# Optimization experiments

Measured on AMD Instinct MI355X. Metric: run time of the kernel, lower is better.

## Reference

```python
import jax, jax.numpy as jnp
import numpy as np

V, H, NH, I, L, P = 32000, 1024, 16, 4096, 8, 2048
B, S = 2, 2048
DH = H // NH
EPS = 1e-5


def setup_inputs() -> dict:
    key = jax.random.key(0)
    ks = jax.random.split(key, 12)
    std = 0.02
    inp = {
        'input_ids': jax.random.randint(ks[0], (B, S), 0, V),
        'attention_mask': jnp.ones((B, S), dtype=jnp.float32),
        'tok_emb': jax.random.normal(ks[1], (V, H), jnp.float32) * std,
        'pos_emb': jax.random.normal(ks[2], (P, H), jnp.float32) * std,
        # per-layer params stacked on leading L dim (torch Linear convention: y = x @ W.T + b)
        'Wq': jax.random.normal(ks[3], (L, H, H), jnp.float32) * std,
        'bq': jnp.zeros((L, H), jnp.float32),
        'Wk': jax.random.normal(ks[4], (L, H, H), jnp.float32) * std,
        'bk': jnp.zeros((L, H), jnp.float32),
        'Wv': jax.random.normal(ks[5], (L, H, H), jnp.float32) * std,
        'bv': jnp.zeros((L, H), jnp.float32),
        'Wi': jax.random.normal(ks[6], (L, I, H), jnp.float32) * std,
        'bi': jnp.zeros((L, I), jnp.float32),
        'Wo': jax.random.normal(ks[7], (L, H, I), jnp.float32) * std,
        'bo': jnp.zeros((L, H), jnp.float32),
        'ln1_g': jnp.ones((L, H), jnp.float32),
        'ln1_b': jnp.zeros((L, H), jnp.float32),
        'ln2_g': jnp.ones((L, H), jnp.float32),
        'ln2_b': jnp.zeros((L, H), jnp.float32),
        'lnf_g': jnp.ones((H,), jnp.float32),
        'lnf_b': jnp.zeros((H,), jnp.float32),
        'Wlm': jax.random.normal(ks[8], (V, H), jnp.float32) * std,
    }
    return inp


def _layer_norm(x, g, b):
    m = jnp.mean(x, axis=-1, keepdims=True)
    v = jnp.var(x, axis=-1, keepdims=True)
    return (x - m) * jax.lax.rsqrt(v + EPS) * g + b


def reference(input_ids, attention_mask, tok_emb, pos_emb, Wq, bq, Wk, bk, Wv, bv,
              Wi, bi, Wo, bo, ln1_g, ln1_b, ln2_g, ln2_b, lnf_g, lnf_b, Wlm):
    b, s = input_ids.shape
    h = tok_emb[input_ids] + pos_emb[jnp.arange(s)][None, :, :]  # [B,S,H]
    mask = (1.0 - attention_mask)[:, None, None, :] * -10000.0   # [B,1,1,S]
    scale = 1.0 / (DH ** 0.5)

    def split_heads(x):  # [B,S,H] -> [B,NH,S,DH]
        return x.reshape(b, s, NH, DH).transpose(0, 2, 1, 3)

    def block(h, p):
        wq, bq_, wk, bk_, wv, bv_, wi, bi_, wo, bo_, g1, b1, g2, b2 = p
        q = split_heads(h @ wq.T + bq_)
        k = split_heads(h @ wk.T + bk_)
        v = split_heads(h @ wv.T + bv_)
        scores = jnp.einsum('bhqd,bhkd->bhqk', q, k) * scale + mask
        probs = jax.nn.softmax(scores, axis=-1)
        ctx = jnp.einsum('bhqk,bhkd->bhqd', probs, v)
        ctx = ctx.transpose(0, 2, 1, 3).reshape(b, s, H)
        h1 = _layer_norm(h + ctx, g1, b1)
        mlp = jax.nn.gelu(h1 @ wi.T + bi_, approximate=False) @ wo.T + bo_
        return _layer_norm(h1 + mlp, g2, b2), None

    h, _ = jax.lax.scan(block, h, (Wq, bq, Wk, bk, Wv, bv, Wi, bi, Wo, bo,
                                   ln1_g, ln1_b, ln2_g, ln2_b))
    h = _layer_norm(h, lnf_g, lnf_b)
    return h @ Wlm.T  # [B,S,V]
```

## Files before the change

### kernel.cpp

```cpp
#include <hip/hip_runtime.h>
#include <hip/hip_bf16.h>

#define V_ 32000
#define H_ 1024
#define NH_ 16
#define I_ 4096
#define L_ 8
#define B_ 2
#define S_ 2048
#define DH_ 64
#define M_ 4096
#define QS_ 3072

typedef __attribute__((ext_vector_type(4))) float f32x4;
typedef __attribute__((ext_vector_type(8))) short s16x8;

#define BARRIER() do { asm volatile("" ::: "memory"); __builtin_amdgcn_s_barrier(); asm volatile("" ::: "memory"); } while (0)
#define SCHEDB()  __builtin_amdgcn_sched_barrier(0)

__device__ __forceinline__ unsigned short f2b(float f) {
  union { float f; unsigned u; } x; x.f = f;
  return (unsigned short)((x.u + 0x7FFFu + ((x.u >> 16) & 1u)) >> 16);
}

__device__ __forceinline__ void gl_lds16(const unsigned short* g, unsigned short* l) {
  __builtin_amdgcn_global_load_lds(
      (__attribute__((address_space(1))) const void*)g,
      (__attribute__((address_space(3))) void*)l, 16, 0, 0);
}

__global__ __launch_bounds__(256) void wcvt(const float* __restrict__ src,
                                            unsigned short* __restrict__ dst) {
  size_t i = ((size_t)blockIdx.x * 256 + threadIdx.x) * 4;
  float4 v = *(const float4*)(src + i);
  ushort4 b;
  b.x = f2b(v.x); b.y = f2b(v.y); b.z = f2b(v.z); b.w = f2b(v.w);
  *(ushort4*)(dst + i) = b;
}

__global__ __launch_bounds__(256) void qkvcat_all(const float* __restrict__ q,
                                                  const float* __restrict__ k,
                                                  const float* __restrict__ v,
                                                  unsigned short* __restrict__ dst) {
  size_t i = ((size_t)blockIdx.x * 256 + threadIdx.x) * 4;
  size_t l = i / (3u * H_ * H_);
  size_t r = i - l * (3u * H_ * H_);
  const float* s; size_t off;
  if (r < (size_t)H_ * H_)          { s = q; off = l * H_ * H_ + r; }
  else if (r < 2u * H_ * H_)        { s = k; off = l * H_ * H_ + r - (size_t)H_ * H_; }
  else                              { s = v; off = l * H_ * H_ + r - 2u * H_ * H_; }
  float4 vv = *(const float4*)(s + off);
  ushort4 b;
  b.x = f2b(vv.x); b.y = f2b(vv.y); b.z = f2b(vv.z); b.w = f2b(vv.w);
  *(ushort4*)(dst + i) = b;
}

__global__ __launch_bounds__(256) void qkvcat(const float* __restrict__ q,
                                              const float* __restrict__ k,
                                              const float* __restrict__ v,
                                              unsigned short* __restrict__ dst) {
  int i = (blockIdx.x * 256 + threadIdx.x) * 4;
  const float* s; int off;
  if (i < H_ * H_)          { s = q; off = i; }
  else if (i < 2 * H_ * H_) { s = k; off = i - H_ * H_; }
  else                      { s = v; off = i - 2 * H_ * H_; }
  float4 vv = *(const float4*)(s + off);
  ushort4 b;
  b.x = f2b(vv.x); b.y = f2b(vv.y); b.z = f2b(vv.z); b.w = f2b(vv.w);
  *(ushort4*)(dst + i) = b;
}

__global__ __launch_bounds__(256) void bcat(const float* __restrict__ bq,
                                            const float* __restrict__ bk,
                                            const float* __restrict__ bv,
                                            float* __restrict__ dst) {
  int i = blockIdx.x * 256 + threadIdx.x;
  int l = i / (3 * H_), r = i - l * 3 * H_;
  int p = r >> 10, c = r & (H_ - 1);
  const float* s = (p == 0) ? bq : ((p == 1) ? bk : bv);
  dst[i] = s[l * H_ + c];
}

__global__ __launch_bounds__(256) void embed_kernel(
    const int* __restrict__ ids, const float* __restrict__ tok,
    const float* __restrict__ pos, float* __restrict__ h,
    unsigned short* __restrict__ xbf)
{
  int row = blockIdx.x;
  int c4 = threadIdx.x;
  int id = ids[row];
  int s = row & (S_ - 1);
  float4 tv = ((const float4*)(tok + (size_t)id * H_))[c4];
  float4 pv = ((const float4*)(pos + (size_t)s * H_))[c4];
  float4 v; v.x = tv.x + pv.x; v.y = tv.y + pv.y; v.z = tv.z + pv.z; v.w = tv.w + pv.w;
  ((float4*)(h + (size_t)row * H_))[c4] = v;
  ushort4 b; b.x = f2b(v.x); b.y = f2b(v.y); b.z = f2b(v.z); b.w = f2b(v.w);
  ((ushort4*)(xbf + (size_t)row * H_))[c4] = b;
}

template<int EPI>
__global__ __launch_bounds__(256) void gemm_bt(
    const unsigned short* __restrict__ A, const unsigned short* __restrict__ Wb,
    const float* __restrict__ bias, float* __restrict__ outf,
    unsigned short* __restrict__ outb, int M, int N, int K, int ksz)
{
  __shared__ unsigned short As[2][128][32];
  __shared__ unsigned short Bs[2][128][32];
  int t = threadIdx.x;
  int lane = t & 63, wid = t >> 6;
  int m0 = blockIdx.x * 128, n0 = blockIdx.y * 128;
  int z = blockIdx.z;
  int koff = z * ksz;
  const float* bz = (z == 0) ? bias : nullptr;
  if (EPI == 0) outf += (size_t)z * M * N;
  int wm = (wid >> 1) * 64, wn = (wid & 1) * 64;
  int fr = lane & 15, hi = lane >> 4;
  int lrow = lane >> 2;
  int lcolsw = (((lane & 3) ^ (lrow & 3)) * 8);
  int ke = ((hi ^ (fr & 3)) * 8);

  f32x4 acc[4][4] = {};

  const unsigned short* Abase = A  + (size_t)(m0 + wid * 32 + lrow) * K + lcolsw;
  const unsigned short* Bbase = Wb + (size_t)(n0 + wid * 32 + lrow) * K + lcolsw;

  auto stage = [&](int s, int k0) {
    gl_lds16(Abase + k0,                  &As[s][wid * 32][0]);
    gl_lds16(Abase + k0 + (size_t)16 * K, &As[s][wid * 32 + 16][0]);
    gl_lds16(Bbase + k0,                  &Bs[s][wid * 32][0]);
    gl_lds16(Bbase + k0 + (size_t)16 * K, &Bs[s][wid * 32 + 16][0]);
  };

  stage(0, koff);

  int cur = 0;
  for (int k0 = koff; k0 < koff + ksz; k0 += 32) {
    asm volatile("s_waitcnt vmcnt(0)" ::: "memory");
    BARRIER();
    if (k0 + 32 < koff + ksz) stage(cur ^ 1, k0 + 32);
    SCHEDB();
    s16x8 af[4], bfr[4];
    #pragma unroll
    for (int i = 0; i < 4; ++i) af[i]  = *(const s16x8*)(&As[cur][wm + i * 16 + fr][ke]);
    #pragma unroll
    for (int j = 0; j < 4; ++j) bfr[j] = *(const s16x8*)(&Bs[cur][wn + j * 16 + fr][ke]);
    #pragma unroll
    for (int i = 0; i < 4; ++i)
      #pragma unroll
      for (int j = 0; j < 4; ++j)
        acc[i][j] = __builtin_amdgcn_mfma_f32_16x16x32_bf16(af[i], bfr[j], acc[i][j], 0, 0, 0);
    cur ^= 1;
  }

  int fq = lane >> 4;
  #pragma unroll
  for (int i = 0; i < 4; ++i) {
    #pragma unroll
    for (int j = 0; j < 4; ++j) {
      #pragma unroll
      for (int r = 0; r < 4; ++r) {
        int row = m0 + wm + i * 16 + fq * 4 + r;
        int col = n0 + wn + j * 16 + fr;
        float v = acc[i][j][r] + (bz ? bz[col] : 0.f);
        if (EPI == 0) {
          outf[(size_t)row * N + col] = v;
        } else if (EPI == 1) {
          float ge = 0.5f * v * (1.0f + erff(v * 0.70710678118f));
          outb[(size_t)row * N + col] = f2b(ge);
        } else {
          outb[(size_t)row * N + col] = f2b(v);
        }
      }
    }
  }
}

template<int EPI>
__global__ __launch_bounds__(512, 2) void gemm256(
    const unsigned short* __restrict__ A, const unsigned short* __restrict__ Wb,
    const float* __restrict__ bias, float* __restrict__ outf,
    unsigned short* __restrict__ outb, int M, int N, int K)
{
  __shared__ unsigned short ASm[2][16384];
  __shared__ unsigned short BSm[2][16384];

  const int t = threadIdx.x;
  const int lane = t & 63, wid = t >> 6;
  const int wm = wid >> 2, wn = wid & 3;
  const int fr = lane & 15, hi = lane >> 4;

  const int Nt = N >> 8;
  const int nwg = gridDim.x;
  const int cpx = nwg >> 3;
  int bid = (int)blockIdx.x;
  int swz = (bid & 7) * cpx + (bid >> 3);
  int band = swz / (4 * Nt);
  int rem = swz - band * (4 * Nt);
  const int m0 = (band * 4 + (rem & 3)) << 8;
  const int n0 = (rem >> 2) << 8;

  const int NT = K >> 6;

  const int srow = lane >> 3;
  const int scol = ((lane & 7) ^ srow) << 3;
  const int ch0 = wid * 2;

  const int axorb = (fr & 7) << 4;
  const int koe0 = ((hi * 16) ^ axorb) >> 1;
  const int koe1 = (((hi * 16) | 64) ^ axorb) >> 1;

  f32x4 acc[8][4] = {};

  auto stage_half = [&](int slot, int h, int k0) {
    if (h < 2) {
      const unsigned short* src =
          A + (size_t)(m0 + h * 128 + ch0 * 8 + srow) * K + k0 + scol;
      unsigned short* dst = &ASm[slot][(h * 128 + ch0 * 8) * 64];
      gl_lds16(src, dst);
      gl_lds16(src + (size_t)8 * K, dst + 8 * 64);
    } else {
      const unsigned short* src =
          Wb + (size_t)(n0 + (h - 2) * 128 + ch0 * 8 + srow) * K + k0 + scol;
      unsigned short* dst = &BSm[slot][((h - 2) * 128 + ch0 * 8) * 64];
      gl_lds16(src, dst);
      gl_lds16(src + (size_t)8 * K, dst + 8 * 64);
    }
  };

  stage_half(0, 2, 0); stage_half(0, 3, 0); stage_half(0, 0, 0); stage_half(0, 1, 0);

  s16x8 af0[4][2], af1[4][2], bfv[4][2];

  for (int T = 0; T < NT; ++T) {
    const int s = T & 1;
    const int k1 = (T + 1) << 6;
    const bool more = (T + 1 < NT);

    asm volatile("s_waitcnt vmcnt(0)" ::: "memory");
    BARRIER();

    const unsigned short* As_ = ASm[s];
    const unsigned short* Bs_ = BSm[s];

    #pragma unroll
    for (int mi = 0; mi < 4; ++mi) {
      const unsigned short* p = As_ + (wm * 128 + mi * 16 + fr) * 64;
      af0[mi][0] = *(const s16x8*)(p + koe0);
      af0[mi][1] = *(const s16x8*)(p + koe1);
    }
    #pragma unroll
    for (int nj = 0; nj < 4; ++nj) {
      const unsigned short* p = Bs_ + (wn * 64 + nj * 16 + fr) * 64;
      bfv[nj][0] = *(const s16x8*)(p + koe0);
      bfv[nj][1] = *(const s16x8*)(p + koe1);
    }
    if (more) stage_half(s ^ 1, 2, k1);
    SCHEDB();
    __builtin_amdgcn_s_setprio(1);
    #pragma unroll
    for (int mi = 0; mi < 4; ++mi)
      #pragma unroll
      for (int nj = 0; nj < 2; ++nj) {
        acc[mi][nj] = __builtin_amdgcn_mfma_f32_16x16x32_bf16(af0[mi][0], bfv[nj][0], acc[mi][nj], 0, 0, 0);
        acc[mi][nj] = __builtin_amdgcn_mfma_f32_16x16x32_bf16(af0[mi][1], bfv[nj][1], acc[mi][nj], 0, 0, 0);
      }
    __builtin_amdgcn_s_setprio(0);
    SCHEDB();

    #pragma unroll
    for (int mi = 0; mi < 4; ++mi) {
      const unsigned short* p = As_ + (wm * 128 + (mi + 4) * 16 + fr) * 64;
      af1[mi][0] = *(const s16x8*)(p + koe0);
      af1[mi][1] = *(const s16x8*)(p + koe1);
    }
    if (more) stage_half(s ^ 1, 3, k1);
    SCHEDB();
    __builtin_amdgcn_s_setprio(1);
    #pragma unroll
    for (int mi = 0; mi < 4; ++mi)
      #pragma unroll
      for (int nj = 2; nj < 4; ++nj) {
        acc[mi][nj] = __builtin_amdgcn_mfma_f32_16x16x32_bf16(af0[mi][0], bfv[nj][0], acc[mi][nj], 0, 0, 0);
        acc[mi][nj] = __builtin_amdgcn_mfma_f32_16x16x32_bf16(af0[mi][1], bfv[nj][1], acc[mi][nj], 0, 0, 0);
      }
    __builtin_amdgcn_s_setprio(0);
    SCHEDB();

    if (more) stage_half(s ^ 1, 0, k1);
    SCHEDB();
    __builtin_amdgcn_s_setprio(1);
    #pragma unroll
    for (int mi = 0; mi < 4; ++mi)
      #pragma unroll
      for (int nj = 2; nj < 4; ++nj) {
        acc[mi + 4][nj] = __builtin_amdgcn_mfma_f32_16x16x32_bf16(af1[mi][0], bfv[nj][0], acc[mi + 4][nj], 0, 0, 0);
        acc[mi + 4][nj] = __builtin_amdgcn_mfma_f32_16x16x32_bf16(af1[mi][1], bfv[nj][1], acc[mi + 4][nj], 0, 0, 0);
      }
    __builtin_amdgcn_s_setprio(0);
    SCHEDB();

    if (more) stage_half(s ^ 1, 1, k1);
    SCHEDB();
    __builtin_amdgcn_s_setprio(1);
    #pragma unroll
    for (int mi = 0; mi < 4; ++mi)
      #pragma unroll
      for (int nj = 0; nj < 2; ++nj) {
        acc[mi + 4][nj] = __builtin_amdgcn_mfma_f32_16x16x32_bf16(af1[mi][0], bfv[nj][0], acc[mi + 4][nj], 0, 0, 0);
        acc[mi + 4][nj] = __builtin_amdgcn_mfma_f32_16x16x32_bf16(af1[mi][1], bfv[nj][1], acc[mi + 4][nj], 0, 0, 0);
      }
    __builtin_amdgcn_s_setprio(0);
  }

  #pragma unroll
  for (int mi = 0; mi < 8; ++mi) {
    #pragma unroll
    for (int nj = 0; nj < 4; ++nj) {
      #pragma unroll
      for (int r = 0; r < 4; ++r) {
        int row = m0 + wm * 128 + mi * 16 + hi * 4 + r;
        int col = n0 + wn * 64 + nj * 16 + fr;
        float v = acc[mi][nj][r] + (bias ? bias[col] : 0.f);
        if (EPI == 0) {
          outf[(size_t)row * N + col] = v;
        } else if (EPI == 1) {
          float ge = 0.5f * v * (1.0f + erff(v * 0.70710678118f));
          outb[(size_t)row * N + col] = f2b(ge);
        } else {
          outb[(size_t)row * N + col] = f2b(v);
        }
      }
    }
  }
}

__global__ __launch_bounds__(256) void transpose_v_bf16(
    const unsigned short* __restrict__ v, unsigned short* __restrict__ vT)
{
  __shared__ unsigned short tile[32][34];
  int bh = blockIdx.z;
  int b = bh >> 4, hh = bh & 15;
  const unsigned short* src = v + (size_t)b * S_ * QS_ + hh * DH_;
  unsigned short* dst = vT + (size_t)bh * DH_ * S_;
  int s0 = blockIdx.x * 32, d0 = blockIdx.y * 32;
  int x = threadIdx.x, y = threadIdx.y;
  #pragma unroll
  for (int i = 0; i < 4; ++i)
    tile[y + i * 8][x] = src[(size_t)(s0 + y + i * 8) * QS_ + d0 + x];
  __syncthreads();
  #pragma unroll
  for (int i = 0; i < 4; ++i)
    dst[(size_t)(d0 + y + i * 8) * S_ + s0 + x] = tile[x][y + i * 8];
}

#define KB_ 64
#define SPL_ 1024
__global__ __launch_bounds__(512) void flash_mfma(
    const unsigned short* __restrict__ qb,
    const unsigned short* __restrict__ kb,
    const unsigned short* __restrict__ vtb,
    const float* __restrict__ mask,
    float* __restrict__ opart,
    float2* __restrict__ ml)
{
  __shared__ unsigned short K2[2][KB_ * DH_];
  __shared__ unsigned short V2[2][DH_ * KB_];
  __shared__ unsigned short Ps[8][16][72];
  __shared__ float xpose[8][16];

  const float LOG2E = 1.4426950408889634f;
  const float SCL = 0.125f * LOG2E;
  int t = threadIdx.x, lane = t & 63, wid = t >> 6;
  int blk = blockIdx.x;
  int bh = blk & 31;
  int rest = blk >> 5;
  int qt = rest & 15, sp = rest >> 4;
  int b = bh >> 4, hh = bh & 15;
  int row0 = b * S_ + qt * 128 + wid * 16;
  int fr = lane & 15, hi = lane >> 4;
  const float* mrow = mask + (size_t)b * S_;
  const int kv0 = sp * SPL_;

  s16x8 qf[2];
  {
    const unsigned short* qrow = qb + (size_t)(row0 + fr) * QS_ + hh * DH_;
    qf[0] = *(const s16x8*)(qrow + hi * 8);
    qf[1] = *(const s16x8*)(qrow + 32 + hi * 8);
  }

  float m_run = -3.0e38f, l_run = 0.f;
  f32x4 octx[4] = {};

  const unsigned short* Kbase = kb + (size_t)b * S_ * QS_ + hh * DH_;
  const unsigned short* Vbase = vtb + (size_t)bh * DH_ * S_;

  int crow = lane >> 3;
  int scol = ((lane & 7) ^ crow) * 8;

  auto stage = [&](int slot, int t0) {
    gl_lds16(Kbase + (size_t)(t0 + wid * 8 + crow) * QS_ + scol, &K2[slot][wid * 512]);
    gl_lds16(Vbase + (size_t)(wid * 8 + crow) * S_ + t0 + scol,  &V2[slot][wid * 512]);
  };

  stage(0, kv0);

  const int swz = (fr & 7) * 8;

  int tt = 0;
  for (int t0 = kv0; t0 < kv0 + SPL_; t0 += KB_, ++tt) {
    int slot = tt & 1;
    __syncthreads();
    if (t0 + KB_ < kv0 + SPL_) stage(slot ^ 1, t0 + KB_);

    f32x4 sacc[4] = {};
    #pragma unroll
    for (int g = 0; g < 4; ++g) {
      #pragma unroll
      for (int i = 0; i < 2; ++i) {
        s16x8 kf = *(const s16x8*)(&K2[slot][(g * 16 + fr) * 64 + ((i * 32 + hi * 8) ^ swz)]);
        sacc[g] = __builtin_amdgcn_mfma_f32_16x16x32_bf16(kf, qf[i], sacc[g], 0, 0, 0);
      }
    }

    float sc[4][4];
    float tm = -3.0e38f;
    #pragma unroll
    for (int g = 0; g < 4; ++g) {
      float4 mq = *(const float4*)(mrow + t0 + g * 16 + hi * 4);
      #pragma unroll
      for (int r = 0; r < 4; ++r) {
        float mk = (1.0f - ((const float*)&mq)[r]) * (-10000.0f * LOG2E);
        float v = sacc[g][r] * SCL + mk;
        sc[g][r] = v;
        tm = fmaxf(tm, v);
      }
    }
    tm = fmaxf(tm, __shfl_xor(tm, 16));
    tm = fmaxf(tm, __shfl_xor(tm, 32));

    if (!__all(tm <= m_run + 8.0f)) {
      float mn = fmaxf(m_run, tm);
      float corr = exp2f(m_run - mn);
      m_run = mn; l_run *= corr;
      xpose[wid][fr] = corr;
      float cr0 = xpose[wid][hi * 4 + 0];
      float cr1 = xpose[wid][hi * 4 + 1];
      float cr2 = xpose[wid][hi * 4 + 2];
      float cr3 = xpose[wid][hi * 4 + 3];
      #pragma unroll
      for (int dg = 0; dg < 4; ++dg) {
        octx[dg][0] *= cr0; octx[dg][1] *= cr1;
        octx[dg][2] *= cr2; octx[dg][3] *= cr3;
      }
    }

    float ps = 0.f;
    #pragma unroll
    for (int g = 0; g < 4; ++g)
      #pragma unroll
      for (int r = 0; r < 4; ++r) {
        float p = exp2f(sc[g][r] - m_run);
        sc[g][r] = p;
        ps += p;
      }
    ps += __shfl_xor(ps, 16);
    ps += __shfl_xor(ps, 32);
    l_run += ps;

    #pragma unroll
    for (int g = 0; g < 4; ++g) {
      uint2 pk;
      pk.x = (unsigned)f2b(sc[g][0]) | ((unsigned)f2b(sc[g][1]) << 16);
      pk.y = (unsigned)f2b(sc[g][2]) | ((unsigned)f2b(sc[g][3]) << 16);
      *(uint2*)(&Ps[wid][fr][g * 16 + hi * 4]) = pk;
    }

    #pragma unroll
    for (int kc = 0; kc < 2; ++kc) {
      s16x8 pf = *(const s16x8*)(&Ps[wid][fr][kc * 32 + hi * 8]);
      #pragma unroll
      for (int dg = 0; dg < 4; ++dg) {
        s16x8 vf2 = *(const s16x8*)(&V2[slot][(dg * 16 + fr) * 64 + ((kc * 32 + hi * 8) ^ swz)]);
        octx[dg] = __builtin_amdgcn_mfma_f32_16x16x32_bf16(pf, vf2, octx[dg], 0, 0, 0);
      }
    }
  }

  float* ob = opart + (size_t)sp * M_ * H_;
  #pragma unroll
  for (int dg = 0; dg < 4; ++dg) {
    size_t base = (size_t)(row0 + hi * 4) * H_ + hh * DH_ + dg * 16 + fr;
    ob[base]          = octx[dg][0];
    ob[base + H_]     = octx[dg][1];
    ob[base + 2 * H_] = octx[dg][2];
    ob[base + 3 * H_] = octx[dg][3];
  }
  if (hi == 0)
    ml[((size_t)sp * 32 + bh) * S_ + qt * 128 + wid * 16 + fr] =
        make_float2(m_run, l_run);
}

__global__ __launch_bounds__(256) void add_ln_mrg(
    const float* __restrict__ x, const float* __restrict__ o0,
    const float* __restrict__ o1, const float2* __restrict__ ml,
    const float* __restrict__ g, const float* __restrict__ bb,
    float* __restrict__ outf, unsigned short* __restrict__ outb)
{
  __shared__ float a1[4], a2[4];
  int row = blockIdx.x, t = threadIdx.x;
  int hh = t >> 4;
  int bh = (row >> 11) * NH_ + hh;
  int q = row & (S_ - 1);
  float2 a = ml[(size_t)bh * S_ + q];
  float2 c = ml[(size_t)(32 + bh) * S_ + q];
  float m = fmaxf(a.x, c.x);
  float w0 = exp2f(a.x - m), w1 = exp2f(c.x - m);
  float inv0 = 1.0f / (a.y * w0 + c.y * w1);
  float4 v  = ((const float4*)(x  + (size_t)row * H_))[t];
  float4 u0 = ((const float4*)(o0 + (size_t)row * H_))[t];
  float4 u1 = ((const float4*)(o1 + (size_t)row * H_))[t];
  v.x += (u0.x * w0 + u1.x * w1) * inv0;
  v.y += (u0.y * w0 + u1.y * w1) * inv0;
  v.z += (u0.z * w0 + u1.z * w1) * inv0;
  v.w += (u0.w * w0 + u1.w * w1) * inv0;
  float s1 = v.x + v.y + v.z + v.w;
  float s2 = v.x * v.x + v.y * v.y + v.z * v.z + v.w * v.w;
  #pragma unroll
  for (int d = 32; d; d >>= 1) { s1 += __shfl_xor(s1, d); s2 += __shfl_xor(s2, d); }
  if ((t & 63) == 0) { a1[t >> 6] = s1; a2[t >> 6] = s2; }
  __syncthreads();
  s1 = a1[0] + a1[1] + a1[2] + a1[3];
  s2 = a2[0] + a2[1] + a2[2] + a2[3];
  float mean = s1 * (1.0f / H_);
  float var = s2 * (1.0f / H_) - mean * mean;
  float inv = rsqrtf(var + 1e-5f);
  float4 gv = ((const float4*)g)[t];
  float4 bv = ((const float4*)bb)[t];
  float4 o;
  o.x = (v.x - mean) * inv * gv.x + bv.x;
  o.y = (v.y - mean) * inv * gv.y + bv.y;
  o.z = (v.z - mean) * inv * gv.z + bv.z;
  o.w = (v.w - mean) * inv * gv.w + bv.w;
  if (outf) ((float4*)(outf + (size_t)row * H_))[t] = o;
  if (outb) {
    ushort4 ob; ob.x = f2b(o.x); ob.y = f2b(o.y); ob.z = f2b(o.z); ob.w = f2b(o.w);
    ((ushort4*)(outb + (size_t)row * H_))[t] = ob;
  }
}

__global__ __launch_bounds__(256) void add_ln(
    const float* __restrict__ x, const float* __restrict__ y,
    const float* __restrict__ y2,
    const float* __restrict__ g, const float* __restrict__ bb,
    float* __restrict__ outf, unsigned short* __restrict__ outb)
{
  __shared__ float a1[4], a2[4];
  int row = blockIdx.x, t = threadIdx.x;
  float4 v = ((const float4*)(x + (size_t)row * H_))[t];
  if (y) {
    float4 u = ((const float4*)(y + (size_t)row * H_))[t];
    v.x += u.x; v.y += u.y; v.z += u.z; v.w += u.w;
  }
  if (y2) {
    float4 u = ((const float4*)(y2 + (size_t)row * H_))[t];
    v.x += u.x; v.y += u.y; v.z += u.z; v.w += u.w;
  }
  float s1 = v.x + v.y + v.z + v.w;
  float s2 = v.x * v.x + v.y * v.y + v.z * v.z + v.w * v.w;
  #pragma unroll
  for (int d = 32; d; d >>= 1) { s1 += __shfl_xor(s1, d); s2 += __shfl_xor(s2, d); }
  if ((t & 63) == 0) { a1[t >> 6] = s1; a2[t >> 6] = s2; }
  __syncthreads();
  s1 = a1[0] + a1[1] + a1[2] + a1[3];
  s2 = a2[0] + a2[1] + a2[2] + a2[3];
  float mean = s1 * (1.0f / H_);
  float var = s2 * (1.0f / H_) - mean * mean;
  float inv = rsqrtf(var + 1e-5f);
  float4 gv = ((const float4*)g)[t];
  float4 bv = ((const float4*)bb)[t];
  float4 o;
  o.x = (v.x - mean) * inv * gv.x + bv.x;
  o.y = (v.y - mean) * inv * gv.y + bv.y;
  o.z = (v.z - mean) * inv * gv.z + bv.z;
  o.w = (v.w - mean) * inv * gv.w + bv.w;
  if (outf) ((float4*)(outf + (size_t)row * H_))[t] = o;
  if (outb) {
    ushort4 ob; ob.x = f2b(o.x); ob.y = f2b(o.y); ob.z = f2b(o.z); ob.w = f2b(o.w);
    ((ushort4*)(outb + (size_t)row * H_))[t] = ob;
  }
}

extern "C" void kernel_launch(void* const* d_in, const int* in_sizes, int n_in,
                              void* d_out, int out_size, void* d_ws, size_t ws_size,
                              hipStream_t stream) {
  const int*   ids  = (const int*)d_in[0];
  const float* mask = (const float*)d_in[1];
  const float* tok  = (const float*)d_in[2];
  const float* pos  = (const float*)d_in[3];
  const float* Wq   = (const float*)d_in[4];
  const float* bq   = (const float*)d_in[5];
  const float* Wk   = (const float*)d_in[6];
  const float* bk   = (const float*)d_in[7];
  const float* Wv   = (const float*)d_in[8];
  const float* bv   = (const float*)d_in[9];
  const float* Wi   = (const float*)d_in[10];
  const float* bi   = (const float*)d_in[11];
  const float* Wo   = (const float*)d_in[12];
  const float* bo   = (const float*)d_in[13];
  const float* ln1g = (const float*)d_in[14];
  const float* ln1b = (const float*)d_in[15];
  const float* ln2g = (const float*)d_in[16];
  const float* ln2b = (const float*)d_in[17];
  const float* lnfg = (const float*)d_in[18];
  const float* lnfb = (const float*)d_in[19];
  const float* Wlm  = (const float*)d_in[20];
  float* out = (float*)d_out;

  char* w = (char*)d_ws;
  size_t off = 0;
  auto alloc = [&](size_t bytes) { void* p = w + off; off = (off + bytes + 255) & ~(size_t)255; return p; };
  float* h     = (float*)alloc((size_t)M_ * H_ * 4);
  unsigned short* qkvb  = (unsigned short*)alloc((size_t)M_ * QS_ * 2);
  unsigned short* vtb   = (unsigned short*)alloc((size_t)B_ * NH_ * DH_ * S_ * 2);
  unsigned short* xbf   = (unsigned short*)alloc((size_t)M_ * H_ * 2);
  unsigned short* midbf = (unsigned short*)alloc((size_t)M_ * I_ * 2);
  float* bqkv  = (float*)alloc((size_t)L_ * QS_ * 4);
  float* opart = (float*)alloc((size_t)2 * M_ * H_ * 4);
  float2* mlbuf = (float2*)alloc((size_t)2 * 32 * S_ * 8);

  size_t wqkv_b = (size_t)L_ * 3 * H_ * H_ * 2;
  size_t wi_bb  = (size_t)L_ * I_ * H_ * 2;
  size_t wo_bb  = (size_t)L_ * H_ * I_ * 2;
  size_t wlm_bb = (size_t)V_ * H_ * 2;
  bool big = (ws_size - off) >= (wqkv_b + wi_bb + wo_bb + wlm_bb + 4 * 256);

  unsigned short *wqkv, *wi_a, *wo_a, *wlm_a, *wbuf = nullptr;
  if (big) {
    wqkv  = (unsigned short*)alloc(wqkv_b);
    wi_a  = (unsigned short*)alloc(wi_bb);
    wo_a  = (unsigned short*)alloc(wo_bb);
    wlm_a = (unsigned short*)alloc(wlm_bb);
    qkvcat_all<<<dim3((unsigned)((size_t)L_ * 3 * H_ * H_ / 1024)), 256, 0, stream>>>(Wq, Wk, Wv, wqkv);
    wcvt<<<dim3((unsigned)((size_t)L_ * I_ * H_ / 1024)), 256, 0, stream>>>(Wi, wi_a);
    wcvt<<<dim3((unsigned)((size_t)L_ * H_ * I_ / 1024)), 256, 0, stream>>>(Wo, wo_a);
    wcvt<<<dim3((unsigned)((size_t)V_ * H_ / 1024)), 256, 0, stream>>>(Wlm, wlm_a);
  } else {
    wbuf = (unsigned short*)alloc((size_t)V_ * H_ * 2);
  }

  bcat<<<dim3(L_ * QS_ / 256), 256, 0, stream>>>(bq, bk, bv, bqkv);
  embed_kernel<<<dim3(M_), 256, 0, stream>>>(ids, tok, pos, h, xbf);

  for (int l = 0; l < L_; ++l) {
    const unsigned short* wq_l;
    if (big) wq_l = wqkv + (size_t)l * 3 * H_ * H_;
    else {
      qkvcat<<<dim3(3 * H_ * H_ / 1024), 256, 0, stream>>>(
          Wq + (size_t)l * H_ * H_, Wk + (size_t)l * H_ * H_, Wv + (size_t)l * H_ * H_, wbuf);
      wq_l = wbuf;
    }
    gemm_bt<2><<<dim3(M_ / 128, QS_ / 128, 1), 256, 0, stream>>>(
        xbf, wq_l, bqkv + (size_t)l * QS_, nullptr, qkvb, M_, QS_, H_, H_);

    transpose_v_bf16<<<dim3(S_ / 32, DH_ / 32, B_ * NH_), dim3(32, 8), 0, stream>>>(
        qkvb + 2 * H_, vtb);
    flash_mfma<<<dim3(B_ * NH_ * S_ / 128 * 2), 512, 0, stream>>>(
        qkvb, qkvb + H_, vtb, mask, opart, mlbuf);

    add_ln_mrg<<<dim3(M_), 256, 0, stream>>>(
        h, opart, opart + (size_t)M_ * H_, mlbuf,
        ln1g + l * H_, ln1b + l * H_, h, xbf);

    const unsigned short* wi_l;
    if (big) wi_l = wi_a + (size_t)l * I_ * H_;
    else {
      wcvt<<<dim3(I_ * H_ / 1024), 256, 0, stream>>>(Wi + (size_t)l * I_ * H_, wbuf);
      wi_l = wbuf;
    }
    gemm256<1><<<dim3((M_ / 256) * (I_ / 256)), 512, 0, stream>>>(
        xbf, wi_l, bi + l * I_, nullptr, midbf, M_, I_, H_);

    const unsigned short* wo_l;
    if (big) wo_l = wo_a + (size_t)l * H_ * I_;
    else {
      wcvt<<<dim3(H_ * I_ / 1024), 256, 0, stream>>>(Wo + (size_t)l * H_ * I_, wbuf);
      wo_l = wbuf;
    }
    gemm_bt<0><<<dim3(M_ / 128, H_ / 128, 2), 256, 0, stream>>>(
        midbf, wo_l, bo + l * H_, opart, nullptr, M_, H_, I_, I_ / 2);

    add_ln<<<dim3(M_), 256, 0, stream>>>(
        h, opart, opart + (size_t)M_ * H_,
        ln2g + l * H_, ln2b + l * H_, h, xbf);
  }

  add_ln<<<dim3(M_), 256, 0, stream>>>(h, nullptr, nullptr, lnfg, lnfb, nullptr, xbf);
  const unsigned short* wlm_l;
  if (big) wlm_l = wlm_a;
  else {
    wcvt<<<dim3(V_ * H_ / 1024), 256, 0, stream>>>(Wlm, wbuf);
    wlm_l = wbuf;
  }
  gemm256<0><<<dim3((M_ / 256) * (V_ / 256)), 512, 0, stream>>>(
      xbf, wlm_l, nullptr, out, nullptr, M_, V_, H_);
}
```

Before: 2.919 ms.

## Restructure GEMM mainloop into 8-wave ping-pong schedule with finer-grained prefetch

Rewrites the bf16 GEMM main loop so global-to-LDS loads are split into per-half A/B stages, with some issued two tiles ahead into the current buffer once its halves are consumed. Each MFMA cluster is bracketed by barriers and an explicit lgkmcnt(0) wait, and vmcnt waits are partial rather than full drains. The aim is to keep more memory traffic in flight across the loop boundary and interleave LDS reads with MFMA more tightly. In exchange it adds several extra workgroup barriers per iteration, which could stall waves, and it depends on exact vmcnt accounting to stay correct.

```diff
diff --git a/kernel.cpp b/kernel.cpp
--- a/kernel.cpp
+++ b/kernel.cpp
@@ -17,6 +17,7 @@
 
 #define BARRIER() do { asm volatile("" ::: "memory"); __builtin_amdgcn_s_barrier(); asm volatile("" ::: "memory"); } while (0)
 #define SCHEDB()  __builtin_amdgcn_sched_barrier(0)
+#define LGKM0()   do { asm volatile("s_waitcnt lgkmcnt(0)" ::: "memory"); __builtin_amdgcn_sched_barrier(0); } while (0)
 
 __device__ __forceinline__ unsigned short f2b(float f) {
   union { float f; unsigned u; } x; x.f = f;
@@ -211,34 +212,36 @@
 
   f32x4 acc[8][4] = {};
 
-  auto stage_half = [&](int slot, int h, int k0) {
-    if (h < 2) {
-      const unsigned short* src =
-          A + (size_t)(m0 + h * 128 + ch0 * 8 + srow) * K + k0 + scol;
-      unsigned short* dst = &ASm[slot][(h * 128 + ch0 * 8) * 64];
-      gl_lds16(src, dst);
-      gl_lds16(src + (size_t)8 * K, dst + 8 * 64);
-    } else {
-      const unsigned short* src =
-          Wb + (size_t)(n0 + (h - 2) * 128 + ch0 * 8 + srow) * K + k0 + scol;
-      unsigned short* dst = &BSm[slot][((h - 2) * 128 + ch0 * 8) * 64];
-      gl_lds16(src, dst);
-      gl_lds16(src + (size_t)8 * K, dst + 8 * 64);
-    }
+  auto stageA = [&](int slot, int h, int T) {
+    const unsigned short* src =
+        A + (size_t)(m0 + h * 128 + ch0 * 8 + srow) * K + (T << 6) + scol;
+    unsigned short* dst = &ASm[slot][(h * 128 + ch0 * 8) * 64];
+    gl_lds16(src, dst);
+    gl_lds16(src + (size_t)8 * K, dst + 8 * 64);
   };
-
-  stage_half(0, 2, 0); stage_half(0, 3, 0); stage_half(0, 0, 0); stage_half(0, 1, 0);
+  auto stageB = [&](int slot, int h, int T) {
+    const unsigned short* src =
+        Wb + (size_t)(n0 + h * 128 + ch0 * 8 + srow) * K + (T << 6) + scol;
+    unsigned short* dst = &BSm[slot][(h * 128 + ch0 * 8) * 64];
+    gl_lds16(src, dst);
+    gl_lds16(src + (size_t)8 * K, dst + 8 * 64);
+  };
+
+  stageB(0, 0, 0); stageA(0, 0, 0); stageB(0, 1, 0); stageA(0, 1, 0);
+  if (NT > 1) {
+    stageB(1, 0, 1); stageA(1, 0, 1);
+    asm volatile("s_waitcnt vmcnt(4)" ::: "memory");
+  } else {
+    asm volatile("s_waitcnt vmcnt(0)" ::: "memory");
+  }
+  BARRIER();
 
   s16x8 af0[4][2], af1[4][2], bfv[4][2];
 
   for (int T = 0; T < NT; ++T) {
     const int s = T & 1;
-    const int k1 = (T + 1) << 6;
-    const bool more = (T + 1 < NT);
-
-    asm volatile("s_waitcnt vmcnt(0)" ::: "memory");
-    BARRIER();
-
+    const bool more1 = (T + 1 < NT);
+    const bool more2 = (T + 2 < NT);
     const unsigned short* As_ = ASm[s];
     const unsigned short* Bs_ = BSm[s];
 
@@ -249,13 +252,14 @@
       af0[mi][1] = *(const s16x8*)(p + koe1);
     }
     #pragma unroll
-    for (int nj = 0; nj < 4; ++nj) {
+    for (int nj = 0; nj < 2; ++nj) {
       const unsigned short* p = Bs_ + (wn * 64 + nj * 16 + fr) * 64;
       bfv[nj][0] = *(const s16x8*)(p + koe0);
       bfv[nj][1] = *(const s16x8*)(p + koe1);
     }
-    if (more) stage_half(s ^ 1, 2, k1);
+    if (more1) stageB(s ^ 1, 1, T + 1);
     SCHEDB();
+    BARRIER(); LGKM0();
     __builtin_amdgcn_s_setprio(1);
     #pragma unroll
     for (int mi = 0; mi < 4; ++mi)
@@ -265,7 +269,27 @@
         acc[mi][nj] = __builtin_amdgcn_mfma_f32_16x16x32_bf16(af0[mi][1], bfv[nj][1], acc[mi][nj], 0, 0, 0);
       }
     __builtin_amdgcn_s_setprio(0);
+    BARRIER();
+
+    #pragma unroll
+    for (int nj = 2; nj < 4; ++nj) {
+      const unsigned short* p = Bs_ + (wn * 64 + nj * 16 + fr) * 64;
+      bfv[nj][0] = *(const s16x8*)(p + koe0);
+      bfv[nj][1] = *(const s16x8*)(p + koe1);
+    }
+    if (more1) stageA(s ^ 1, 1, T + 1);
     SCHEDB();
+    BARRIER(); LGKM0();
+    __builtin_amdgcn_s_setprio(1);
+    #pragma unroll
+    for (int mi = 0; mi < 4; ++mi)
+      #pragma unroll
+      for (int nj = 2; nj < 4; ++nj) {
+        acc[mi][nj] = __builtin_amdgcn_mfma_f32_16x16x32_bf16(af0[mi][0], bfv[nj][0], acc[mi][nj], 0, 0, 0);
+        acc[mi][nj] = __builtin_amdgcn_mfma_f32_16x16x32_bf16(af0[mi][1], bfv[nj][1], acc[mi][nj], 0, 0, 0);
+      }
+    __builtin_amdgcn_s_setprio(0);
+    BARRIER();
 
     #pragma unroll
     for (int mi = 0; mi < 4; ++mi) {
@@ -273,21 +297,9 @@
       af1[mi][0] = *(const s16x8*)(p + koe0);
       af1[mi][1] = *(const s16x8*)(p + koe1);
     }
-    if (more) stage_half(s ^ 1, 3, k1);
+    if (more2) stageB(s, 0, T + 2);
     SCHEDB();
-    __builtin_amdgcn_s_setprio(1);
-    #pragma unroll
-    for (int mi = 0; mi < 4; ++mi)
-      #pragma unroll
-      for (int nj = 2; nj < 4; ++nj) {
-        acc[mi][nj] = __builtin_amdgcn_mfma_f32_16x16x32_bf16(af0[mi][0], bfv[nj][0], acc[mi][nj], 0, 0, 0);
-        acc[mi][nj] = __builtin_amdgcn_mfma_f32_16x16x32_bf16(af0[mi][1], bfv[nj][1], acc[mi][nj], 0, 0, 0);
-      }
-    __builtin_amdgcn_s_setprio(0);
-    SCHEDB();
-
-    if (more) stage_half(s ^ 1, 0, k1);
-    SCHEDB();
+    BARRIER(); LGKM0();
     __builtin_amdgcn_s_setprio(1);
     #pragma unroll
     for (int mi = 0; mi < 4; ++mi)
@@ -297,9 +309,9 @@
         acc[mi + 4][nj] = __builtin_amdgcn_mfma_f32_16x16x32_bf16(af1[mi][1], bfv[nj][1], acc[mi + 4][nj], 0, 0, 0);
       }
     __builtin_amdgcn_s_setprio(0);
-    SCHEDB();
-
-    if (more) stage_half(s ^ 1, 1, k1);
+    BARRIER();
+
+    if (more2) stageA(s, 0, T + 2);
     SCHEDB();
     __builtin_amdgcn_s_setprio(1);
     #pragma unroll
@@ -310,6 +322,11 @@
         acc[mi + 4][nj] = __builtin_amdgcn_mfma_f32_16x16x32_bf16(af1[mi][1], bfv[nj][1], acc[mi + 4][nj], 0, 0, 0);
       }
     __builtin_amdgcn_s_setprio(0);
+    if (more1) {
+      if (more2) asm volatile("s_waitcnt vmcnt(4)" ::: "memory");
+      else       asm volatile("s_waitcnt vmcnt(0)" ::: "memory");
+      BARRIER();
+    }
   }
 
   #pragma unroll
```

New measurement: 2.886 ms. No clear change (-1.1%).

## Switch 256x256 GEMM to triple-buffered K=32 stages with prefetch distance two

Applied to the files above, without the earlier changes.

The 256x256 GEMM kernel moves from a double-buffered K=64 tile with a split half-stage schedule to a triple-buffered K=32 tile that prefetches two stages ahead and waits with a partial vmcnt. The goal is to keep global loads in flight across a whole iteration instead of draining all loads before each barrier. LDS use drops from 128 KB to 96 KB, the occupancy hint of two blocks is removed, and the swizzle is simplified for 32-wide rows. In exchange there are twice as many barriers per K, and the fine interleaving of loads with MFMA groups is gone.

```diff
diff --git a/kernel.cpp b/kernel.cpp
--- a/kernel.cpp
+++ b/kernel.cpp
@@ -176,13 +176,13 @@
 }
 
 template<int EPI>
-__global__ __launch_bounds__(512, 2) void gemm256(
+__global__ __launch_bounds__(512) void gemm256(
     const unsigned short* __restrict__ A, const unsigned short* __restrict__ Wb,
     const float* __restrict__ bias, float* __restrict__ outf,
     unsigned short* __restrict__ outb, int M, int N, int K)
 {
-  __shared__ unsigned short ASm[2][16384];
-  __shared__ unsigned short BSm[2][16384];
+  __shared__ unsigned short ASm[3][8192];
+  __shared__ unsigned short BSm[3][8192];
 
   const int t = threadIdx.x;
   const int lane = t & 63, wid = t >> 6;
@@ -199,116 +199,55 @@
   const int m0 = (band * 4 + (rem & 3)) << 8;
   const int n0 = (rem >> 2) << 8;
 
-  const int NT = K >> 6;
-
-  const int srow = lane >> 3;
-  const int scol = ((lane & 7) ^ srow) << 3;
-  const int ch0 = wid * 2;
-
-  const int axorb = (fr & 7) << 4;
-  const int koe0 = ((hi * 16) ^ axorb) >> 1;
-  const int koe1 = (((hi * 16) | 64) ^ axorb) >> 1;
+  const int NT = K >> 5;
+
+  const int srow = lane >> 2;
+  const int scol = ((lane & 3) ^ (srow & 3)) * 8;
+  const int ke = ((hi ^ (fr & 3)) * 8);
 
   f32x4 acc[8][4] = {};
 
-  auto stage_half = [&](int slot, int h, int k0) {
-    if (h < 2) {
-      const unsigned short* src =
-          A + (size_t)(m0 + h * 128 + ch0 * 8 + srow) * K + k0 + scol;
-      unsigned short* dst = &ASm[slot][(h * 128 + ch0 * 8) * 64];
-      gl_lds16(src, dst);
-      gl_lds16(src + (size_t)8 * K, dst + 8 * 64);
-    } else {
-      const unsigned short* src =
-          Wb + (size_t)(n0 + (h - 2) * 128 + ch0 * 8 + srow) * K + k0 + scol;
-      unsigned short* dst = &BSm[slot][((h - 2) * 128 + ch0 * 8) * 64];
-      gl_lds16(src, dst);
-      gl_lds16(src + (size_t)8 * K, dst + 8 * 64);
+  auto stage = [&](int slot, int T) {
+    const int kb = T << 5;
+    #pragma unroll
+    for (int h = 0; h < 2; ++h) {
+      const unsigned short* srcA =
+          A + (size_t)(m0 + h * 128 + wid * 16 + srow) * K + kb + scol;
+      gl_lds16(srcA, &ASm[slot][(h * 128 + wid * 16) * 32]);
+      const unsigned short* srcB =
+          Wb + (size_t)(n0 + h * 128 + wid * 16 + srow) * K + kb + scol;
+      gl_lds16(srcB, &BSm[slot][(h * 128 + wid * 16) * 32]);
     }
   };
 
-  stage_half(0, 2, 0); stage_half(0, 3, 0); stage_half(0, 0, 0); stage_half(0, 1, 0);
-
-  s16x8 af0[4][2], af1[4][2], bfv[4][2];
+  stage(0, 0);
+  if (NT > 1) stage(1, 1);
 
   for (int T = 0; T < NT; ++T) {
-    const int s = T & 1;
-    const int k1 = (T + 1) << 6;
-    const bool more = (T + 1 < NT);
-
-    asm volatile("s_waitcnt vmcnt(0)" ::: "memory");
+    const int s = T % 3;
+    if (T + 1 < NT) { asm volatile("s_waitcnt vmcnt(4)" ::: "memory"); }
+    else            { asm volatile("s_waitcnt vmcnt(0)" ::: "memory"); }
     BARRIER();
+    if (T + 2 < NT) stage((T + 2) % 3, T + 2);
+    SCHEDB();
 
     const unsigned short* As_ = ASm[s];
     const unsigned short* Bs_ = BSm[s];
 
-    #pragma unroll
-    for (int mi = 0; mi < 4; ++mi) {
-      const unsigned short* p = As_ + (wm * 128 + mi * 16 + fr) * 64;
-      af0[mi][0] = *(const s16x8*)(p + koe0);
-      af0[mi][1] = *(const s16x8*)(p + koe1);
-    }
-    #pragma unroll
-    for (int nj = 0; nj < 4; ++nj) {
-      const unsigned short* p = Bs_ + (wn * 64 + nj * 16 + fr) * 64;
-      bfv[nj][0] = *(const s16x8*)(p + koe0);
-      bfv[nj][1] = *(const s16x8*)(p + koe1);
-    }
-    if (more) stage_half(s ^ 1, 2, k1);
-    SCHEDB();
+    s16x8 af[8], bfr[4];
+    #pragma unroll
+    for (int nj = 0; nj < 4; ++nj)
+      bfr[nj] = *(const s16x8*)(Bs_ + (wn * 64 + nj * 16 + fr) * 32 + ke);
+    #pragma unroll
+    for (int mi = 0; mi < 8; ++mi)
+      af[mi] = *(const s16x8*)(As_ + (wm * 128 + mi * 16 + fr) * 32 + ke);
+
     __builtin_amdgcn_s_setprio(1);
     #pragma unroll
-    for (int mi = 0; mi < 4; ++mi)
-      #pragma unroll
-      for (int nj = 0; nj < 2; ++nj) {
-        acc[mi][nj] = __builtin_amdgcn_mfma_f32_16x16x32_bf16(af0[mi][0], bfv[nj][0], acc[mi][nj], 0, 0, 0);
-        acc[mi][nj] = __builtin_amdgcn_mfma_f32_16x16x32_bf16(af0[mi][1], bfv[nj][1], acc[mi][nj], 0, 0, 0);
-      }
-    __builtin_amdgcn_s_setprio(0);
-    SCHEDB();
-
-    #pragma unroll
-    for (int mi = 0; mi < 4; ++mi) {
-      const unsigned short* p = As_ + (wm * 128 + (mi + 4) * 16 + fr) * 64;
-      af1[mi][0] = *(const s16x8*)(p + koe0);
-      af1[mi][1] = *(const s16x8*)(p + koe1);
-    }
-    if (more) stage_half(s ^ 1, 3, k1);
-    SCHEDB();
-    __builtin_amdgcn_s_setprio(1);
-    #pragma unroll
-    for (int mi = 0; mi < 4; ++mi)
-      #pragma unroll
-      for (int nj = 2; nj < 4; ++nj) {
-        acc[mi][nj] = __builtin_amdgcn_mfma_f32_16x16x32_bf16(af0[mi][0], bfv[nj][0], acc[mi][nj], 0, 0, 0);
-        acc[mi][nj] = __builtin_amdgcn_mfma_f32_16x16x32_bf16(af0[mi][1], bfv[nj][1], acc[mi][nj], 0, 0, 0);
-      }
-    __builtin_amdgcn_s_setprio(0);
-    SCHEDB();
-
-    if (more) stage_half(s ^ 1, 0, k1);
-    SCHEDB();
-    __builtin_amdgcn_s_setprio(1);
-    #pragma unroll
-    for (int mi = 0; mi < 4; ++mi)
-      #pragma unroll
-      for (int nj = 2; nj < 4; ++nj) {
-        acc[mi + 4][nj] = __builtin_amdgcn_mfma_f32_16x16x32_bf16(af1[mi][0], bfv[nj][0], acc[mi + 4][nj], 0, 0, 0);
-        acc[mi + 4][nj] = __builtin_amdgcn_mfma_f32_16x16x32_bf16(af1[mi][1], bfv[nj][1], acc[mi + 4][nj], 0, 0, 0);
-      }
-    __builtin_amdgcn_s_setprio(0);
-    SCHEDB();
-
-    if (more) stage_half(s ^ 1, 1, k1);
-    SCHEDB();
-    __builtin_amdgcn_s_setprio(1);
-    #pragma unroll
-    for (int mi = 0; mi < 4; ++mi)
-      #pragma unroll
-      for (int nj = 0; nj < 2; ++nj) {
-        acc[mi + 4][nj] = __builtin_amdgcn_mfma_f32_16x16x32_bf16(af1[mi][0], bfv[nj][0], acc[mi + 4][nj], 0, 0, 0);
-        acc[mi + 4][nj] = __builtin_amdgcn_mfma_f32_16x16x32_bf16(af1[mi][1], bfv[nj][1], acc[mi + 4][nj], 0, 0, 0);
-      }
+    for (int mi = 0; mi < 8; ++mi)
+      #pragma unroll
+      for (int nj = 0; nj < 4; ++nj)
+        acc[mi][nj] = __builtin_amdgcn_mfma_f32_16x16x32_bf16(af[mi], bfr[nj], acc[mi][nj], 0, 0, 0);
     __builtin_amdgcn_s_setprio(0);
   }
 
```

After: 3.087 ms. +5.7%, slower.
